# Performance work log

Measured on AMD Instinct MI355X. Metric: run time of the kernel, lower is better.

## Reference

```python
import jax, jax.numpy as jnp
import numpy as np

_W1 = np.array([[[-1, 0, 0], [0, 1, 0], [0, 0, 0]],
                [[0, -1, 0], [0, 1, 0], [0, 0, 0]],
                [[0, 0, -1], [0, 1, 0], [0, 0, 0]],
                [[0, 0, 0], [-1, 1, 0], [0, 0, 0]]], dtype=np.float32).reshape(4, 1, 3, 3)
_W2 = _W1[:, :, ::-1, ::-1].copy()

BN_EPS = 1e-3  # YOLOX BaseConv BatchNorm eps
SHIFTS = (1, 3)


def _conv1x1(x, w, b=None):
    # x: (B,C,H,W), w: (O,C,1,1)
    y = jnp.einsum('bchw,oc->bohw', x, w[:, :, 0, 0])
    if b is not None:
        y = y + b[None, :, None, None]
    return y


def _grouped_dilated(x, w, d, groups):
    # 3x3 grouped conv, dilation d, 'same' padding (pad = d for 3x3)
    return jax.lax.conv_general_dilated(
        x, w, window_strides=(1, 1), padding=((d, d), (d, d)),
        rhs_dilation=(d, d), dimension_numbers=('NCHW', 'OIHW', 'NCHW'),
        feature_group_count=groups)


def setup_inputs() -> dict:
    key = jax.random.key(0)
    ks = jax.random.split(key, 6)
    B, C, H, W = 4, 128, 384, 384
    Cq = C // 4
    return {
        'cen': jax.random.normal(ks[0], (B, C, H, W), jnp.float32),
        'mas': jax.random.normal(ks[1], (B, 1, H, W), jnp.float32),
        'scales': jnp.zeros((4,), jnp.float32),
        'in_conv_w': jax.random.normal(ks[2], (Cq, C, 1, 1), jnp.float32) * 0.05,
        'in_conv_b': jnp.zeros((Cq,), jnp.float32),
        'base_w': jax.random.normal(ks[3], (Cq, Cq, 1, 1), jnp.float32) * 0.1,
        'bn_gamma': jnp.ones((Cq,), jnp.float32),
        'bn_beta': jnp.zeros((Cq,), jnp.float32),
        'bn_mean': jnp.zeros((Cq,), jnp.float32),
        'bn_var': jnp.ones((Cq,), jnp.float32),
        'out_w': jax.random.normal(ks[4], (1, Cq, 1, 1), jnp.float32) * 0.1,
        'out_b': jnp.zeros((1,), jnp.float32),
    }


def reference(cen, mas, scales, in_conv_w, in_conv_b, base_w,
              bn_gamma, bn_beta, bn_mean, bn_var, out_w, out_b):
    B, C, H, W = cen.shape
    Cq = C // 4
    k1 = jnp.asarray(np.tile(_W1, (Cq, 1, 1, 1)))  # (4*Cq,1,3,3)
    k2 = jnp.asarray(np.tile(_W2, (Cq, 1, 1, 1)))

    x = _conv1x1(cen, in_conv_w, in_conv_b)  # (B,Cq,H,W)
    outs = []
    for shift in SHIFTS:
        o1 = _grouped_dilated(x, k1, shift, Cq)  # (B,4*Cq,H,W)
        o2 = _grouped_dilated(x, k2, shift, Cq)
        o = (o1 * o2).reshape(B, Cq, 4, H, W).min(axis=2)
        outs.append(o)
    outs = jnp.stack(outs, axis=-1)  # (B,Cq,H,W,n_shifts)
    feat = jax.nn.relu(outs.max(axis=-1) + outs.mean(axis=-1))

    # out_conv = BaseConv(1x1, BN, SiLU) + Conv2d(Cq->1, 1x1)
    y = _conv1x1(feat, base_w)
    inv = jax.lax.rsqrt(bn_var + BN_EPS)
    y = (y - bn_mean[None, :, None, None]) * (bn_gamma * inv)[None, :, None, None] + bn_beta[None, :, None, None]
    y = jax.nn.silu(y)
    att = jax.nn.sigmoid(_conv1x1(y, out_w, out_b))  # (B,1,H,W)

    s = jax.nn.softmax(scales)
    m = jax.nn.sigmoid(mas)
    return cen * (att * m * s[0] + m * s[1] + s[2] * att + s[3])
```

## Files before the change

kernel.cpp:

```cpp
#include <hip/hip_runtime.h>

#define HH 384
#define WW 384
#define HWSZ (HH*WW)
#define CIN 128
#define CQ 32
#define NB 4
#define NPIX (NB*HWSZ)

__device__ __forceinline__ float sigmoidf_(float v){ return 1.0f/(1.0f + __expf(-v)); }

__global__ __launch_bounds__(256) void k_conv1(const float* __restrict__ cen,
    const float* __restrict__ wmat, const float* __restrict__ bvec,
    float* __restrict__ x) {
  __shared__ float wl[CIN*CQ];
  int t = threadIdx.x;
  for (int i = t; i < CIN*CQ; i += 256) {
    int c = i >> 5, o = i & 31;
    wl[i] = wmat[o*CIN + c];
  }
  __syncthreads();
  int p0  = blockIdx.x * 512 + t;
  int b   = p0 / HWSZ;
  int pix = p0 - b*HWSZ;
  const float* cb = cen + (size_t)b*CIN*HWSZ + pix;
  float acc0[CQ], acc1[CQ];
  #pragma unroll
  for (int o=0;o<CQ;o++){ acc0[o]=0.f; acc1[o]=0.f; }
  for (int c=0;c<CIN;c++){
    float v0 = cb[(size_t)c*HWSZ];
    float v1 = cb[(size_t)c*HWSZ + 256];
    #pragma unroll
    for (int o=0;o<CQ;o++){
      float wv = wl[c*CQ + o];
      acc0[o] += v0*wv;
      acc1[o] += v1*wv;
    }
  }
  float* xb = x + (size_t)b*CQ*HWSZ + pix;
  #pragma unroll
  for (int o=0;o<CQ;o++){
    float bb = bvec[o];
    xb[(size_t)o*HWSZ]       = acc0[o] + bb;
    xb[(size_t)o*HWSZ + 256] = acc1[o] + bb;
  }
}

__global__ __launch_bounds__(256) void k_att(const float* __restrict__ x,
    const float* __restrict__ mas, const float* __restrict__ scales,
    const float* __restrict__ base_w,
    const float* __restrict__ bn_g, const float* __restrict__ bn_b,
    const float* __restrict__ bn_m, const float* __restrict__ bn_v,
    const float* __restrict__ out_w, const float* __restrict__ out_b,
    float* __restrict__ a_out) {
  __shared__ float bwl[CQ*CQ];
  __shared__ float ows[CQ], bns[CQ], bnsh[CQ];
  int t = threadIdx.x;
  for (int i=t;i<CQ*CQ;i+=256) bwl[i] = base_w[i];
  if (t < CQ) {
    float inv = rsqrtf(bn_v[t] + 1e-3f);
    float g = bn_g[t]*inv;
    bns[t]  = g;
    bnsh[t] = bn_b[t] - bn_m[t]*g;
    ows[t]  = out_w[t];
  }
  __syncthreads();
  int p   = blockIdx.x*256 + t;
  int b   = p / HWSZ;
  int pix = p - b*HWSZ;
  int h   = pix / WW;
  int w   = pix - h*WW;

  const int dh[17] = {0, -1,1,-1,1,-1,1, 0,0, -3,3,-3,3,-3,3, 0,0};
  const int dw[17] = {0, -1,1, 0,0, 1,-1,-1,1, -3,3, 0,0, 3,-3,-3,3};
  int   idx[17]; float flg[17];
  #pragma unroll
  for (int k=0;k<17;k++){
    int hh = h + dh[k], wq = w + dw[k];
    bool ok = ((unsigned)hh < (unsigned)HH) && ((unsigned)wq < (unsigned)WW);
    int hc = min(max(hh,0),HH-1), wc = min(max(wq,0),WW-1);
    idx[k] = hc*WW + wc;
    flg[k] = ok ? 1.0f : 0.0f;
  }

  const float* xb = x + (size_t)b*CQ*HWSZ;
  float feat[CQ];
  #pragma unroll
  for (int c=0;c<CQ;c++){
    const float* xc = xb + (size_t)c*HWSZ;
    float xv = xc[idx[0]];
    float n[17];
    #pragma unroll
    for (int k=1;k<17;k++) n[k] = xc[idx[k]] * flg[k];
    float q0 = (xv-n[1])*(xv-n[2]);
    float q1 = (xv-n[3])*(xv-n[4]);
    float q2 = (xv-n[5])*(xv-n[6]);
    float q3 = (xv-n[7])*(xv-n[8]);
    float os0 = fminf(fminf(q0,q1),fminf(q2,q3));
    float r0 = (xv-n[9])*(xv-n[10]);
    float r1 = (xv-n[11])*(xv-n[12]);
    float r2 = (xv-n[13])*(xv-n[14]);
    float r3 = (xv-n[15])*(xv-n[16]);
    float os1 = fminf(fminf(r0,r1),fminf(r2,r3));
    float v = fmaxf(os0,os1) + 0.5f*(os0+os1);
    feat[c] = fmaxf(v, 0.0f);
  }

  float att_lin = out_b[0];
  #pragma unroll
  for (int o=0;o<CQ;o++){
    float y = 0.f;
    #pragma unroll
    for (int c=0;c<CQ;c++) y += feat[c]*bwl[o*CQ+c];
    y = y*bns[o] + bnsh[o];
    att_lin += ows[o]*(y*sigmoidf_(y));
  }
  float att = sigmoidf_(att_lin);

  float s0=scales[0],s1=scales[1],s2=scales[2],s3=scales[3];
  float mx = fmaxf(fmaxf(s0,s1),fmaxf(s2,s3));
  float e0=__expf(s0-mx), e1=__expf(s1-mx), e2=__expf(s2-mx), e3=__expf(s3-mx);
  float inv = 1.0f/(e0+e1+e2+e3);
  float m = sigmoidf_(mas[p]);
  a_out[p] = (att*m)*(e0*inv) + m*(e1*inv) + att*(e2*inv) + (e3*inv);
}

__global__ __launch_bounds__(256) void k_out(const float* __restrict__ cen,
    const float* __restrict__ a, float* __restrict__ out){
  unsigned i = blockIdx.x*256u + threadIdx.x;
  unsigned e = i*4u;
  unsigned bc  = e / HWSZ;
  unsigned pix = e - bc*HWSZ;
  unsigned b   = bc >> 7;
  float4 v  = ((const float4*)cen)[i];
  float4 av = ((const float4*)a)[(b*HWSZ + pix) >> 2];
  float4 r;
  r.x = v.x*av.x; r.y = v.y*av.y; r.z = v.z*av.z; r.w = v.w*av.w;
  ((float4*)out)[i] = r;
}

extern "C" void kernel_launch(void* const* d_in, const int* in_sizes, int n_in,
                              void* d_out, int out_size, void* d_ws, size_t ws_size,
                              hipStream_t stream) {
  const float* cen    = (const float*)d_in[0];
  const float* mas    = (const float*)d_in[1];
  const float* scales = (const float*)d_in[2];
  const float* in_w   = (const float*)d_in[3];
  const float* in_b   = (const float*)d_in[4];
  const float* base_w = (const float*)d_in[5];
  const float* bn_g   = (const float*)d_in[6];
  const float* bn_b   = (const float*)d_in[7];
  const float* bn_m   = (const float*)d_in[8];
  const float* bn_v   = (const float*)d_in[9];
  const float* out_w  = (const float*)d_in[10];
  const float* out_b  = (const float*)d_in[11];
  float* out = (float*)d_out;

  float* x = (float*)d_ws;
  float* a = x + (size_t)NB*CQ*HWSZ;

  k_conv1<<<NPIX/512, 256, 0, stream>>>(cen, in_w, in_b, x);
  k_att  <<<NPIX/256, 256, 0, stream>>>(x, mas, scales, base_w,
                                        bn_g, bn_b, bn_m, bn_v, out_w, out_b, a);
  k_out  <<<(NB*CIN*HWSZ)/1024, 256, 0, stream>>>(cen, a, out);
}
```

Baseline: 748.1 us.

## Tile stencil kernel through LDS and vectorize 1x1 conv loads

The attention kernel now handles a 4x64 pixel tile per block. For each channel it stages a haloed 10x70 region into double-buffered shared memory, so neighbours come from LDS instead of 17 scattered global loads per pixel, and the 32x32 projection is accumulated per channel so the feature array no longer has to be held. The input conv now loads two adjacent pixels as float2 and unrolls by four channels. This adds one block barrier per channel and more register pressure in the conv kernel.

```diff
diff --git a/kernel.cpp b/kernel.cpp
--- a/kernel.cpp
+++ b/kernel.cpp
@@ -20,31 +20,44 @@
     wl[i] = wmat[o*CIN + c];
   }
   __syncthreads();
-  int p0  = blockIdx.x * 512 + t;
+  int p0  = blockIdx.x * 512 + t*2;
   int b   = p0 / HWSZ;
   int pix = p0 - b*HWSZ;
   const float* cb = cen + (size_t)b*CIN*HWSZ + pix;
-  float acc0[CQ], acc1[CQ];
+  float2 acc[CQ];
   #pragma unroll
-  for (int o=0;o<CQ;o++){ acc0[o]=0.f; acc1[o]=0.f; }
-  for (int c=0;c<CIN;c++){
-    float v0 = cb[(size_t)c*HWSZ];
-    float v1 = cb[(size_t)c*HWSZ + 256];
+  for (int o=0;o<CQ;o++){ acc[o].x=0.f; acc[o].y=0.f; }
+  #pragma unroll 2
+  for (int c=0;c<CIN;c+=4){
+    float2 v0 = *(const float2*)(cb + (size_t)(c+0)*HWSZ);
+    float2 v1 = *(const float2*)(cb + (size_t)(c+1)*HWSZ);
+    float2 v2 = *(const float2*)(cb + (size_t)(c+2)*HWSZ);
+    float2 v3 = *(const float2*)(cb + (size_t)(c+3)*HWSZ);
     #pragma unroll
     for (int o=0;o<CQ;o++){
-      float wv = wl[c*CQ + o];
-      acc0[o] += v0*wv;
-      acc1[o] += v1*wv;
+      float w0 = wl[(c+0)*CQ+o], w1 = wl[(c+1)*CQ+o];
+      float w2 = wl[(c+2)*CQ+o], w3 = wl[(c+3)*CQ+o];
+      acc[o].x = fmaf(v0.x,w0,acc[o].x); acc[o].y = fmaf(v0.y,w0,acc[o].y);
+      acc[o].x = fmaf(v1.x,w1,acc[o].x); acc[o].y = fmaf(v1.y,w1,acc[o].y);
+      acc[o].x = fmaf(v2.x,w2,acc[o].x); acc[o].y = fmaf(v2.y,w2,acc[o].y);
+      acc[o].x = fmaf(v3.x,w3,acc[o].x); acc[o].y = fmaf(v3.y,w3,acc[o].y);
     }
   }
   float* xb = x + (size_t)b*CQ*HWSZ + pix;
   #pragma unroll
   for (int o=0;o<CQ;o++){
     float bb = bvec[o];
-    xb[(size_t)o*HWSZ]       = acc0[o] + bb;
-    xb[(size_t)o*HWSZ + 256] = acc1[o] + bb;
+    float2 r; r.x = acc[o].x + bb; r.y = acc[o].y + bb;
+    *(float2*)(xb + (size_t)o*HWSZ) = r;
   }
 }
+
+#define TH 4
+#define TW 64
+#define LDSW 72
+#define LDSN 720
+#define GBX 6
+#define GBY 96
 
 __global__ __launch_bounds__(256) void k_att(const float* __restrict__ x,
     const float* __restrict__ mas, const float* __restrict__ scales,
@@ -55,6 +68,7 @@
     float* __restrict__ a_out) {
   __shared__ float bwl[CQ*CQ];
   __shared__ float ows[CQ], bns[CQ], bnsh[CQ];
+  __shared__ float tile[2][LDSN];
   int t = threadIdx.x;
   for (int i=t;i<CQ*CQ;i+=256) bwl[i] = base_w[i];
   if (t < CQ) {
@@ -64,56 +78,69 @@
     bnsh[t] = bn_b[t] - bn_m[t]*g;
     ows[t]  = out_w[t];
   }
-  __syncthreads();
-  int p   = blockIdx.x*256 + t;
-  int b   = p / HWSZ;
-  int pix = p - b*HWSZ;
-  int h   = pix / WW;
-  int w   = pix - h*WW;
 
-  const int dh[17] = {0, -1,1,-1,1,-1,1, 0,0, -3,3,-3,3,-3,3, 0,0};
-  const int dw[17] = {0, -1,1, 0,0, 1,-1,-1,1, -3,3, 0,0, 3,-3,-3,3};
-  int   idx[17]; float flg[17];
+  int gid = blockIdx.x;
+  int b   = gid / (GBX*GBY);
+  int rem = gid - b*(GBX*GBY);
+  int ty  = rem / GBX;
+  int tx  = rem - ty*GBX;
+  int h0  = ty*TH, w0 = tx*TW;
+
+  int soff[3]; float sval[3];
   #pragma unroll
-  for (int k=0;k<17;k++){
-    int hh = h + dh[k], wq = w + dw[k];
-    bool ok = ((unsigned)hh < (unsigned)HH) && ((unsigned)wq < (unsigned)WW);
-    int hc = min(max(hh,0),HH-1), wc = min(max(wq,0),WW-1);
-    idx[k] = hc*WW + wc;
-    flg[k] = ok ? 1.0f : 0.0f;
+  for (int j=0;j<3;j++){
+    int i = t + j*256;
+    int r = i / LDSW, cc = i - r*LDSW;
+    int hh = h0 - 3 + r, wq = w0 - 3 + cc;
+    bool ok = (i < LDSN) && (cc < 70) &&
+              ((unsigned)hh < (unsigned)HH) && ((unsigned)wq < (unsigned)WW);
+    soff[j] = ok ? (hh*WW + wq) : 0;
+    sval[j] = ok ? 1.0f : 0.0f;
   }
 
+  int rr  = t >> 6, cc2 = t & 63;
+  const int cbase = (3+rr)*LDSW + 3 + cc2;
   const float* xb = x + (size_t)b*CQ*HWSZ;
-  float feat[CQ];
+
+  float y[CQ];
   #pragma unroll
+  for (int o=0;o<CQ;o++) y[o] = 0.f;
+
+  __syncthreads();
+
+  #pragma unroll 2
   for (int c=0;c<CQ;c++){
+    float* buf = tile[c&1];
     const float* xc = xb + (size_t)c*HWSZ;
-    float xv = xc[idx[0]];
-    float n[17];
     #pragma unroll
-    for (int k=1;k<17;k++) n[k] = xc[idx[k]] * flg[k];
-    float q0 = (xv-n[1])*(xv-n[2]);
-    float q1 = (xv-n[3])*(xv-n[4]);
-    float q2 = (xv-n[5])*(xv-n[6]);
-    float q3 = (xv-n[7])*(xv-n[8]);
+    for (int j=0;j<3;j++){
+      int i = t + j*256;
+      if (i < LDSN) buf[i] = sval[j] * xc[soff[j]];
+    }
+    __syncthreads();
+    const float* p = buf + cbase;
+    float xv = p[0];
+    float q0 = (xv-p[-LDSW-1])*(xv-p[ LDSW+1]);
+    float q1 = (xv-p[-LDSW  ])*(xv-p[ LDSW  ]);
+    float q2 = (xv-p[-LDSW+1])*(xv-p[ LDSW-1]);
+    float q3 = (xv-p[-1     ])*(xv-p[ 1     ]);
     float os0 = fminf(fminf(q0,q1),fminf(q2,q3));
-    float r0 = (xv-n[9])*(xv-n[10]);
-    float r1 = (xv-n[11])*(xv-n[12]);
-    float r2 = (xv-n[13])*(xv-n[14]);
-    float r3 = (xv-n[15])*(xv-n[16]);
+    float r0 = (xv-p[-3*LDSW-3])*(xv-p[ 3*LDSW+3]);
+    float r1 = (xv-p[-3*LDSW  ])*(xv-p[ 3*LDSW  ]);
+    float r2 = (xv-p[-3*LDSW+3])*(xv-p[ 3*LDSW-3]);
+    float r3 = (xv-p[-3      ])*(xv-p[ 3       ]);
     float os1 = fminf(fminf(r0,r1),fminf(r2,r3));
     float v = fmaxf(os0,os1) + 0.5f*(os0+os1);
-    feat[c] = fmaxf(v, 0.0f);
+    float fc = fmaxf(v, 0.0f);
+    #pragma unroll
+    for (int o=0;o<CQ;o++) y[o] = fmaf(fc, bwl[o*CQ+c], y[o]);
   }
 
   float att_lin = out_b[0];
   #pragma unroll
   for (int o=0;o<CQ;o++){
-    float y = 0.f;
-    #pragma unroll
-    for (int c=0;c<CQ;c++) y += feat[c]*bwl[o*CQ+c];
-    y = y*bns[o] + bnsh[o];
-    att_lin += ows[o]*(y*sigmoidf_(y));
+    float yy = y[o]*bns[o] + bnsh[o];
+    att_lin += ows[o]*(yy*sigmoidf_(yy));
   }
   float att = sigmoidf_(att_lin);
 
@@ -121,8 +148,9 @@
   float mx = fmaxf(fmaxf(s0,s1),fmaxf(s2,s3));
   float e0=__expf(s0-mx), e1=__expf(s1-mx), e2=__expf(s2-mx), e3=__expf(s3-mx);
   float inv = 1.0f/(e0+e1+e2+e3);
-  float m = sigmoidf_(mas[p]);
-  a_out[p] = (att*m)*(e0*inv) + m*(e1*inv) + att*(e2*inv) + (e3*inv);
+  int p_out = b*HWSZ + (h0+rr)*WW + (w0+cc2);
+  float m = sigmoidf_(mas[p_out]);
+  a_out[p_out] = (att*m)*(e0*inv) + m*(e1*inv) + att*(e2*inv) + (e3*inv);
 }
 
 __global__ __launch_bounds__(256) void k_out(const float* __restrict__ cen,
@@ -160,7 +188,7 @@
   float* a = x + (size_t)NB*CQ*HWSZ;
 
   k_conv1<<<NPIX/512, 256, 0, stream>>>(cen, in_w, in_b, x);
-  k_att  <<<NPIX/256, 256, 0, stream>>>(x, mas, scales, base_w,
-                                        bn_g, bn_b, bn_m, bn_v, out_w, out_b, a);
+  k_att  <<<NB*GBX*GBY, 256, 0, stream>>>(x, mas, scales, base_w,
+                                          bn_g, bn_b, bn_m, bn_v, out_w, out_b, a);
   k_out  <<<(NB*CIN*HWSZ)/1024, 256, 0, stream>>>(cen, a, out);
 }
```

Result: faster. 725.3 us (-3.0%).
